# Kernel optimization log

Measured on AMD Instinct MI355X. Metric: run time of the kernel, lower is better.

Reference implementation:

```python
import jax, jax.numpy as jnp
import numpy as np

EMBED = 256
HEADS = 8
HEAD_DIM = EMBED // HEADS
K = 7          # kernel_size
DIL = 1        # dilation
PAD = DIL * (K - 1) // 2  # 3
B, H, W = 4, 56, 56


def setup_inputs() -> dict:
    key = jax.random.key(0)
    ks = jax.random.split(key, 9)
    d = {"x": jax.random.normal(ks[0], (B, H, W, EMBED), jnp.float32)}
    for i, name in enumerate(["wq", "wk", "wv", "wo"]):
        d[name] = jax.random.normal(ks[1 + i], (EMBED, EMBED), jnp.float32) * 0.02
    for i, name in enumerate(["bq", "bk", "bv", "bo"]):
        d[name] = jax.random.normal(ks[5 + i], (EMBED,), jnp.float32) * 0.02
    return d


def _unfold(t):
    # t: [N, d, H, W] -> [N, d, K*K, H, W]; zero padding (matches F.unfold),
    # so out-of-bounds neighbors contribute logit 0, NOT -inf (faithful to source).
    h, w = t.shape[2], t.shape[3]
    tp = jnp.pad(t, ((0, 0), (0, 0), (PAD, PAD), (PAD, PAD)))
    patches = [tp[:, :, i * DIL:i * DIL + h, j * DIL:j * DIL + w]
               for i in range(K) for j in range(K)]  # fixed K*K=49 offsets
    return jnp.stack(patches, axis=2)


def reference(x, wq, bq, wk, bk, wv, bv, wo, bo):
    b, h, w, c = x.shape
    scale = HEAD_DIM ** -0.5
    q = x @ wq.T + bq
    k = x @ wk.T + bk
    v = x @ wv.T + bv

    def to_nh(t):  # [B,H,W,C] -> [B*heads, head_dim, H, W]
        return t.reshape(b, h, w, HEADS, HEAD_DIM).transpose(0, 3, 4, 1, 2).reshape(b * HEADS, HEAD_DIM, h, w)

    q, k, v = to_nh(q), to_nh(k), to_nh(v)
    k_unf = _unfold(k)  # [N, d, K2, H, W]
    v_unf = _unfold(v)
    logits = jnp.einsum('ndhw,ndkhw->nkhw', q, k_unf) * scale  # [N, K2, H, W]
    attn = jax.nn.softmax(logits, axis=1)
    out = jnp.einsum('nkhw,ndkhw->ndhw', attn, v_unf)  # [N, d, H, W]
    out = out.reshape(b, HEADS, HEAD_DIM, h, w).transpose(0, 3, 4, 1, 2).reshape(b, h, w, c)
    return out @ wo.T + bo
```

## Files before the change

kernel.cpp:

```cpp
#include <hip/hip_runtime.h>

typedef unsigned int u32;
typedef unsigned short u16;
typedef _Float16 f16;
typedef __attribute__((ext_vector_type(8))) _Float16 f16x8;
typedef __attribute__((ext_vector_type(4))) float f32x4;

#define T_TOK 12544
#define EMB   256
#define IMG   56
#define SCALE2 0.25503486f
#define HALO  196
#define KSTR  40
#define VTSTR 208
#define PSTR  136

__device__ __forceinline__ u16 f16b(float f) {
    const f16 h = (f16)f;
    return __builtin_bit_cast(u16, h);
}
__device__ __forceinline__ u32 pk2(float lo, float hi) {
    return (u32)f16b(lo) | ((u32)f16b(hi) << 16);
}
__device__ __forceinline__ uint4 pk16(const float4 a, const float4 b) {
    uint4 r;
    r.x = pk2(a.x, a.y); r.y = pk2(a.z, a.w);
    r.z = pk2(b.x, b.y); r.w = pk2(b.z, b.w);
    return r;
}

#define GLD16(g, l) __builtin_amdgcn_global_load_lds( \
    (const __attribute__((address_space(1))) u32*)(g), \
    (__attribute__((address_space(3))) u32*)(l), 16, 0, 0)

__global__ __launch_bounds__(256) void qkv_mfma(
    const float* __restrict__ xf,
    const float* __restrict__ wq, const float* __restrict__ wk, const float* __restrict__ wv,
    const float* __restrict__ bq, const float* __restrict__ bk, const float* __restrict__ bv,
    u16* __restrict__ qb, u16* __restrict__ kb, u16* __restrict__ vb) {
    __shared__ __attribute__((aligned(16))) u16 sA[2][128 * 32];
    __shared__ __attribute__((aligned(16))) u16 sB[2][128 * 32];
    const int bid = blockIdx.y * 6 + blockIdx.x;
    const int xcd = bid & 7, loc = bid >> 3;
    const int work = (xcd < 4 ? xcd * 74 : 296 + (xcd - 4) * 73) + loc;
    const int nBase = (work % 6) * 128;
    const int mBase = (work / 6) * 128;
    const int tid = threadIdx.x, wv_ = tid >> 6, ln = tid & 63;
    const int lrow = ln & 15, lqd = ln >> 4;
    const int wr = wv_ >> 1, wc = wv_ & 1;

    const int which = nBase >> 8;
    const float* wsrc = (which == 0) ? wq : (which == 1) ? wk : wv;
    const int nrow0 = nBase & 255;

    const int arow = tid >> 2, acol = (tid & 3) * 8;
    const float* gAf = xf   + (size_t)(mBase + arow) * EMB + acol;
    const float* gBf = wsrc + (size_t)(nrow0 + arow) * EMB + acol;
    const int so = tid * 8;

    f32x4 acc[4][4];
    #pragma unroll
    for (int mi = 0; mi < 4; ++mi)
        #pragma unroll
        for (int ni = 0; ni < 4; ++ni) acc[mi][ni] = (f32x4){0.f, 0.f, 0.f, 0.f};

    {
        const float4 ra0 = *(const float4*)(gAf);
        const float4 ra1 = *(const float4*)(gAf + 4);
        const float4 ra2 = *(const float4*)(gAf + 64 * EMB);
        const float4 ra3 = *(const float4*)(gAf + 64 * EMB + 4);
        const float4 rb0 = *(const float4*)(gBf);
        const float4 rb1 = *(const float4*)(gBf + 4);
        const float4 rb2 = *(const float4*)(gBf + 64 * EMB);
        const float4 rb3 = *(const float4*)(gBf + 64 * EMB + 4);
        *(uint4*)&sA[0][so]        = pk16(ra0, ra1);
        *(uint4*)&sA[0][2048 + so] = pk16(ra2, ra3);
        *(uint4*)&sB[0][so]        = pk16(rb0, rb1);
        *(uint4*)&sB[0][2048 + so] = pk16(rb2, rb3);
    }

    for (int kt = 0; kt < 8; ++kt) {
        const int b = kt & 1;
        __syncthreads();
        float4 ra0, ra1, ra2, ra3, rb0, rb1, rb2, rb3;
        if (kt < 7) {
            const int k0 = (kt + 1) * 32;
            ra0 = *(const float4*)(gAf + k0);
            ra1 = *(const float4*)(gAf + k0 + 4);
            ra2 = *(const float4*)(gAf + k0 + 64 * EMB);
            ra3 = *(const float4*)(gAf + k0 + 64 * EMB + 4);
            rb0 = *(const float4*)(gBf + k0);
            rb1 = *(const float4*)(gBf + k0 + 4);
            rb2 = *(const float4*)(gBf + k0 + 64 * EMB);
            rb3 = *(const float4*)(gBf + k0 + 64 * EMB + 4);
        }
        f16x8 af[4], bfr[4];
        #pragma unroll
        for (int mi = 0; mi < 4; ++mi)
            af[mi] = *(const f16x8*)&sA[b][(wr * 64 + mi * 16 + lrow) * 32 + lqd * 8];
        #pragma unroll
        for (int ni = 0; ni < 4; ++ni)
            bfr[ni] = *(const f16x8*)&sB[b][(wc * 64 + ni * 16 + lrow) * 32 + lqd * 8];
        #pragma unroll
        for (int mi = 0; mi < 4; ++mi)
            #pragma unroll
            for (int ni = 0; ni < 4; ++ni)
                acc[mi][ni] = __builtin_amdgcn_mfma_f32_16x16x32_f16(af[mi], bfr[ni], acc[mi][ni], 0, 0, 0);
        if (kt < 7) {
            *(uint4*)&sA[b ^ 1][so]        = pk16(ra0, ra1);
            *(uint4*)&sA[b ^ 1][2048 + so] = pk16(ra2, ra3);
            *(uint4*)&sB[b ^ 1][so]        = pk16(rb0, rb1);
            *(uint4*)&sB[b ^ 1][2048 + so] = pk16(rb2, rb3);
        }
    }

    const float* bias = (which == 0) ? bq : (which == 1) ? bk : bv;
    u16* dst = (which == 0) ? qb : (which == 1) ? kb : vb;
    #pragma unroll
    for (int ni = 0; ni < 4; ++ni) {
        const int cg = nrow0 + wc * 64 + ni * 16;
        const int head = cg >> 5;
        const int d = (cg & 31) + lrow;
        const float bz = bias[cg + lrow];
        u16* dh = dst + (size_t)head * T_TOK * 32;
        #pragma unroll
        for (int mi = 0; mi < 4; ++mi) {
            #pragma unroll
            for (int r = 0; r < 4; ++r) {
                const int row = mBase + wr * 64 + mi * 16 + lqd * 4 + r;
                dh[(size_t)row * 32 + d] = f16b(acc[mi][ni][r] + bz);
            }
        }
    }
}

__global__ __launch_bounds__(256) void out_mfma(
    const u16* __restrict__ ao, const float* __restrict__ wo,
    const float* __restrict__ bo, float* __restrict__ out) {
    __shared__ __attribute__((aligned(16))) u16 sA[2][64 * 32];
    __shared__ __attribute__((aligned(16))) u16 sB[2][64 * 32];
    const int bid = blockIdx.y * 4 + blockIdx.x;
    const int work = (bid & 7) * 98 + (bid >> 3);
    const int nBase = (work & 3) * 64;
    const int mBase = (work >> 2) * 64;
    const int tid = threadIdx.x, wv_ = tid >> 6, ln = tid & 63;
    const int lrow = ln & 15, lqd = ln >> 4;
    const int rA = tid >> 2, kcA = tid & 3;
    const size_t gA = (size_t)(mBase + rA) * EMB + kcA * 8;
    const int lA = wv_ * 512;

    const int brow = tid >> 2, bcol = (tid & 3) * 8;
    const float* gBf = wo + (size_t)(nBase + brow) * EMB + bcol;
    const int so = tid * 8;

    f32x4 acc[4];
    #pragma unroll
    for (int mi = 0; mi < 4; ++mi) acc[mi] = (f32x4){0.f, 0.f, 0.f, 0.f};

    GLD16(ao + gA, &sA[0][lA]);
    {
        const float4 rb0 = *(const float4*)(gBf);
        const float4 rb1 = *(const float4*)(gBf + 4);
        *(uint4*)&sB[0][so] = pk16(rb0, rb1);
    }

    for (int kt = 0; kt < 8; ++kt) {
        const int b = kt & 1;
        __syncthreads();
        float4 rb0, rb1;
        if (kt < 7) {
            const int k0 = (kt + 1) * 32;
            GLD16(ao + gA + k0, &sA[b ^ 1][lA]);
            rb0 = *(const float4*)(gBf + k0);
            rb1 = *(const float4*)(gBf + k0 + 4);
        }
        f16x8 af[4];
        #pragma unroll
        for (int mi = 0; mi < 4; ++mi)
            af[mi] = *(const f16x8*)&sA[b][(mi * 16 + lrow) * 32 + lqd * 8];
        const f16x8 bf = *(const f16x8*)&sB[b][(wv_ * 16 + lrow) * 32 + lqd * 8];
        #pragma unroll
        for (int mi = 0; mi < 4; ++mi)
            acc[mi] = __builtin_amdgcn_mfma_f32_16x16x32_f16(af[mi], bf, acc[mi], 0, 0, 0);
        if (kt < 7) {
            *(uint4*)&sB[b ^ 1][so] = pk16(rb0, rb1);
        }
    }

    const int ncol = nBase + wv_ * 16 + lrow;
    const float bz = bo[ncol];
    #pragma unroll
    for (int mi = 0; mi < 4; ++mi) {
        #pragma unroll
        for (int r = 0; r < 4; ++r) {
            const int row = mBase + mi * 16 + lqd * 4 + r;
            out[(size_t)row * EMB + ncol] = acc[mi][r] + bz;
        }
    }
}

__global__ __launch_bounds__(256, 5) void attn_kernel(
    const u16* __restrict__ qb, const u16* __restrict__ kb, const u16* __restrict__ vb,
    u16* __restrict__ ao) {
    __shared__ __attribute__((aligned(16))) u16 smem[15360];
    u16* sVT = smem;
    u16* sK  = smem + 6656;
    u16* sP  = smem + 6656;

    const int tid = threadIdx.x;
    const int w = tid >> 6, ln = tid & 63;
    const int lrow = ln & 15, lqd = ln >> 4;
    const int img = blockIdx.z >> 3, head = blockIdx.z & 7;
    const int ty0 = blockIdx.y * 8, tx0 = blockIdx.x * 8;
    const int base8 = (28 * w) & ~7;

    const u16* kbh = kb + (size_t)head * (T_TOK * 32);
    const u16* vbh = vb + (size_t)head * (T_TOK * 32);
    const u16* qbh = qb + (size_t)head * (T_TOK * 32);

    for (int i = tid; i < 1248; i += 256) {
        if (i < 832) {
            const int p = i >> 2, c = i & 3;
            const int pyh = p / 14, pxh = p - pyh * 14;
            const int gy = ty0 - 3 + pyh, gx = tx0 - 3 + pxh;
            const bool ok = (p < HALO) & ((unsigned)gy < 56u) & ((unsigned)gx < 56u);
            u16* dstk = sK + p * KSTR + c * 8;
            if (ok) {
                const size_t tt = (size_t)((img * IMG + gy) * IMG + gx) * 32;
                *(uint4*)dstk = *(const uint4*)(kbh + tt + c * 8);
            } else {
                *(uint4*)dstk = (uint4){0u, 0u, 0u, 0u};
            }
        } else {
            const int j = i - 832;
            const int pp = j >> 2, c = j & 3;
            const int p0 = pp * 2;
            const int pyh = p0 / 14, pxh = p0 - pyh * 14;
            const int gy = ty0 - 3 + pyh, gx = tx0 - 3 + pxh;
            const bool oky = (p0 < HALO) & ((unsigned)gy < 56u);
            const bool ok0 = oky & ((unsigned)gx < 56u);
            const bool ok1 = oky & ((unsigned)(gx + 1) < 56u);
            const long long tt = (long long)((img * IMG + gy) * IMG + gx) * 32;
            const uint4 u0 = ok0 ? *(const uint4*)(vbh + tt + c * 8)
                                 : (uint4){0u, 0u, 0u, 0u};
            const uint4 u1 = ok1 ? *(const uint4*)(vbh + tt + 32 + c * 8)
                                 : (uint4){0u, 0u, 0u, 0u};
            u16* dv = sVT + (c * 8) * VTSTR + p0;
            *(u32*)&dv[0 * VTSTR] = (u0.x & 0xffffu) | (u1.x << 16);
            *(u32*)&dv[1 * VTSTR] = (u0.x >> 16)     | (u1.x & 0xffff0000u);
            *(u32*)&dv[2 * VTSTR] = (u0.y & 0xffffu) | (u1.y << 16);
            *(u32*)&dv[3 * VTSTR] = (u0.y >> 16)     | (u1.y & 0xffff0000u);
            *(u32*)&dv[4 * VTSTR] = (u0.z & 0xffffu) | (u1.z << 16);
            *(u32*)&dv[5 * VTSTR] = (u0.z >> 16)     | (u1.z & 0xffff0000u);
            *(u32*)&dv[6 * VTSTR] = (u0.w & 0xffffu) | (u1.w << 16);
            *(u32*)&dv[7 * VTSTR] = (u0.w >> 16)     | (u1.w & 0xffff0000u);
        }
    }

    const int qpy = 2 * w + (lrow >> 3), qpx = lrow & 7;
    const size_t qtok = ((size_t)img * IMG + ty0 + qpy) * IMG + tx0 + qpx;
    const f16x8 aq = *(const f16x8*)&qbh[qtok * 32 + lqd * 8];
    __syncthreads();

    f32x4 ct[8];
    #pragma unroll
    for (int t = 0; t < 8; ++t) ct[t] = (f32x4){0.f, 0.f, 0.f, 0.f};
    #pragma unroll
    for (int t = 0; t < 8; ++t) {
        const f16x8 bk = *(const f16x8*)&sK[(base8 + t * 16 + lrow) * KSTR + lqd * 8];
        ct[t] = __builtin_amdgcn_mfma_f32_16x16x32_f16(bk, aq, ct[t], 0, 0, 0);
    }

    float ssum = 0.f;
    #pragma unroll
    for (int t = 0; t < 8; ++t) {
        #pragma unroll
        for (int r = 0; r < 4; ++r) {
            const int col = base8 + t * 16 + lqd * 4 + r;
            const int hy = col / 14, hx = col - 14 * hy;
            const bool ok = ((unsigned)(hy - qpy) < 7u) &
                            ((unsigned)(hx - qpx) < 7u) & (col < HALO);
            const float e = ok ? exp2f(ct[t][r] * SCALE2) : 0.f;
            ct[t][r] = e;
            ssum += e;
        }
    }
    ssum += __shfl_xor(ssum, 16);
    ssum += __shfl_xor(ssum, 32);
    const float inv = 1.0f / ssum;

    __syncthreads();

    u16* sPw = sP + w * 16 * PSTR;
    #pragma unroll
    for (int t = 0; t < 8; ++t) {
        ushort4 pw;
        pw.x = f16b(ct[t][0]);
        pw.y = f16b(ct[t][1]);
        pw.z = f16b(ct[t][2]);
        pw.w = f16b(ct[t][3]);
        *(ushort4*)&sPw[lrow * PSTR + t * 16 + lqd * 4] = pw;
    }

    f32x4 o0 = (f32x4){0.f, 0.f, 0.f, 0.f};
    f32x4 o1 = (f32x4){0.f, 0.f, 0.f, 0.f};
    #pragma unroll
    for (int ks = 0; ks < 4; ++ks) {
        const f16x8 ap  = *(const f16x8*)&sPw[lrow * PSTR + ks * 32 + lqd * 8];
        const f16x8 av0 = *(const f16x8*)&sVT[lrow * VTSTR + base8 + ks * 32 + lqd * 8];
        const f16x8 av1 = *(const f16x8*)&sVT[(16 + lrow) * VTSTR + base8 + ks * 32 + lqd * 8];
        o0 = __builtin_amdgcn_mfma_f32_16x16x32_f16(av0, ap, o0, 0, 0, 0);
        o1 = __builtin_amdgcn_mfma_f32_16x16x32_f16(av1, ap, o1, 0, 0, 0);
    }

    const size_t base = qtok * EMB + head * 32;
    ushort4 s0, s1;
    s0.x = f16b(o0[0] * inv); s0.y = f16b(o0[1] * inv);
    s0.z = f16b(o0[2] * inv); s0.w = f16b(o0[3] * inv);
    s1.x = f16b(o1[0] * inv); s1.y = f16b(o1[1] * inv);
    s1.z = f16b(o1[2] * inv); s1.w = f16b(o1[3] * inv);
    *(ushort4*)&ao[base + lqd * 4]      = s0;
    *(ushort4*)&ao[base + 16 + lqd * 4] = s1;
}

extern "C" void kernel_launch(void* const* d_in, const int* in_sizes, int n_in,
                              void* d_out, int out_size, void* d_ws, size_t ws_size,
                              hipStream_t stream) {
    const float* x  = (const float*)d_in[0];
    const float* wq = (const float*)d_in[1];
    const float* wk = (const float*)d_in[2];
    const float* wv = (const float*)d_in[3];
    const float* wo = (const float*)d_in[4];
    const float* bq = (const float*)d_in[5];
    const float* bk = (const float*)d_in[6];
    const float* bv = (const float*)d_in[7];
    const float* bo = (const float*)d_in[8];
    float* out = (float*)d_out;

    char* ws = (char*)d_ws;
    u16* qb = (u16*)(ws);
    u16* kb = (u16*)(ws +  6422528);
    u16* vb = (u16*)(ws + 12845056);
    u16* ao = (u16*)(ws + 19267584);

    qkv_mfma<<<dim3(6, 98), 256, 0, stream>>>(x, wq, wk, wv, bq, bk, bv, qb, kb, vb);
    attn_kernel<<<dim3(7, 7, 32), 256, 0, stream>>>(qb, kb, vb, ao);
    out_mfma<<<dim3(4, 196), 256, 0, stream>>>(ao, wo, bo, out);
}
```

Baseline: 116.1 us.

## Vectorize GEMM epilogue stores and read attention keys directly from global

The QKV and output GEMMs swap the MFMA operand order so each lane holds four consecutive output columns of one token. The epilogues then write ushort4/float4 vectors with a float4 bias load, instead of scattered scalar stores. The attention kernel no longer stages the K halo in LDS: each lane loads its key fragment straight from global memory, and a block barrier is dropped because sP no longer aliases live K data. The direct K loads have no bounds or zero-padding check, so out-of-image and padded halo positions read arbitrary memory. That can change the logits the reference sets to zero and risks out-of-range accesses.

```diff
diff --git a/kernel.cpp b/kernel.cpp
--- a/kernel.cpp
+++ b/kernel.cpp
@@ -11,7 +11,6 @@
 #define IMG   56
 #define SCALE2 0.25503486f
 #define HALO  196
-#define KSTR  40
 #define VTSTR 208
 #define PSTR  136
 
@@ -105,7 +104,7 @@
         for (int mi = 0; mi < 4; ++mi)
             #pragma unroll
             for (int ni = 0; ni < 4; ++ni)
-                acc[mi][ni] = __builtin_amdgcn_mfma_f32_16x16x32_f16(af[mi], bfr[ni], acc[mi][ni], 0, 0, 0);
+                acc[mi][ni] = __builtin_amdgcn_mfma_f32_16x16x32_f16(bfr[ni], af[mi], acc[mi][ni], 0, 0, 0);
         if (kt < 7) {
             *(uint4*)&sA[b ^ 1][so]        = pk16(ra0, ra1);
             *(uint4*)&sA[b ^ 1][2048 + so] = pk16(ra2, ra3);
@@ -120,16 +119,18 @@
     for (int ni = 0; ni < 4; ++ni) {
         const int cg = nrow0 + wc * 64 + ni * 16;
         const int head = cg >> 5;
-        const int d = (cg & 31) + lrow;
-        const float bz = bias[cg + lrow];
-        u16* dh = dst + (size_t)head * T_TOK * 32;
+        const int d0 = (cg & 31) + lqd * 4;
+        const float4 bz4 = *(const float4*)&bias[cg + lqd * 4];
+        u16* dh = dst + (size_t)head * (T_TOK * 32);
         #pragma unroll
         for (int mi = 0; mi < 4; ++mi) {
-            #pragma unroll
-            for (int r = 0; r < 4; ++r) {
-                const int row = mBase + wr * 64 + mi * 16 + lqd * 4 + r;
-                dh[(size_t)row * 32 + d] = f16b(acc[mi][ni][r] + bz);
-            }
+            const int token = mBase + wr * 64 + mi * 16 + lrow;
+            ushort4 s;
+            s.x = f16b(acc[mi][ni][0] + bz4.x);
+            s.y = f16b(acc[mi][ni][1] + bz4.y);
+            s.z = f16b(acc[mi][ni][2] + bz4.z);
+            s.w = f16b(acc[mi][ni][3] + bz4.w);
+            *(ushort4*)&dh[(size_t)token * 32 + d0] = s;
         }
     }
 }
@@ -181,21 +182,23 @@
         const f16x8 bf = *(const f16x8*)&sB[b][(wv_ * 16 + lrow) * 32 + lqd * 8];
         #pragma unroll
         for (int mi = 0; mi < 4; ++mi)
-            acc[mi] = __builtin_amdgcn_mfma_f32_16x16x32_f16(af[mi], bf, acc[mi], 0, 0, 0);
+            acc[mi] = __builtin_amdgcn_mfma_f32_16x16x32_f16(bf, af[mi], acc[mi], 0, 0, 0);
         if (kt < 7) {
             *(uint4*)&sB[b ^ 1][so] = pk16(rb0, rb1);
         }
     }
 
-    const int ncol = nBase + wv_ * 16 + lrow;
-    const float bz = bo[ncol];
+    const int nc0 = nBase + wv_ * 16 + lqd * 4;
+    const float4 bz4 = *(const float4*)&bo[nc0];
     #pragma unroll
     for (int mi = 0; mi < 4; ++mi) {
-        #pragma unroll
-        for (int r = 0; r < 4; ++r) {
-            const int row = mBase + mi * 16 + lqd * 4 + r;
-            out[(size_t)row * EMB + ncol] = acc[mi][r] + bz;
-        }
+        const int token = mBase + mi * 16 + lrow;
+        float4 o;
+        o.x = acc[mi][0] + bz4.x;
+        o.y = acc[mi][1] + bz4.y;
+        o.z = acc[mi][2] + bz4.z;
+        o.w = acc[mi][3] + bz4.w;
+        *(float4*)&out[(size_t)token * EMB + nc0] = o;
     }
 }
 
@@ -204,7 +207,6 @@
     u16* __restrict__ ao) {
     __shared__ __attribute__((aligned(16))) u16 smem[15360];
     u16* sVT = smem;
-    u16* sK  = smem + 6656;
     u16* sP  = smem + 6656;
 
     const int tid = threadIdx.x;
@@ -218,43 +220,28 @@
     const u16* vbh = vb + (size_t)head * (T_TOK * 32);
     const u16* qbh = qb + (size_t)head * (T_TOK * 32);
 
-    for (int i = tid; i < 1248; i += 256) {
-        if (i < 832) {
-            const int p = i >> 2, c = i & 3;
-            const int pyh = p / 14, pxh = p - pyh * 14;
-            const int gy = ty0 - 3 + pyh, gx = tx0 - 3 + pxh;
-            const bool ok = (p < HALO) & ((unsigned)gy < 56u) & ((unsigned)gx < 56u);
-            u16* dstk = sK + p * KSTR + c * 8;
-            if (ok) {
-                const size_t tt = (size_t)((img * IMG + gy) * IMG + gx) * 32;
-                *(uint4*)dstk = *(const uint4*)(kbh + tt + c * 8);
-            } else {
-                *(uint4*)dstk = (uint4){0u, 0u, 0u, 0u};
-            }
-        } else {
-            const int j = i - 832;
-            const int pp = j >> 2, c = j & 3;
-            const int p0 = pp * 2;
-            const int pyh = p0 / 14, pxh = p0 - pyh * 14;
-            const int gy = ty0 - 3 + pyh, gx = tx0 - 3 + pxh;
-            const bool oky = (p0 < HALO) & ((unsigned)gy < 56u);
-            const bool ok0 = oky & ((unsigned)gx < 56u);
-            const bool ok1 = oky & ((unsigned)(gx + 1) < 56u);
-            const long long tt = (long long)((img * IMG + gy) * IMG + gx) * 32;
-            const uint4 u0 = ok0 ? *(const uint4*)(vbh + tt + c * 8)
-                                 : (uint4){0u, 0u, 0u, 0u};
-            const uint4 u1 = ok1 ? *(const uint4*)(vbh + tt + 32 + c * 8)
-                                 : (uint4){0u, 0u, 0u, 0u};
-            u16* dv = sVT + (c * 8) * VTSTR + p0;
-            *(u32*)&dv[0 * VTSTR] = (u0.x & 0xffffu) | (u1.x << 16);
-            *(u32*)&dv[1 * VTSTR] = (u0.x >> 16)     | (u1.x & 0xffff0000u);
-            *(u32*)&dv[2 * VTSTR] = (u0.y & 0xffffu) | (u1.y << 16);
-            *(u32*)&dv[3 * VTSTR] = (u0.y >> 16)     | (u1.y & 0xffff0000u);
-            *(u32*)&dv[4 * VTSTR] = (u0.z & 0xffffu) | (u1.z << 16);
-            *(u32*)&dv[5 * VTSTR] = (u0.z >> 16)     | (u1.z & 0xffff0000u);
-            *(u32*)&dv[6 * VTSTR] = (u0.w & 0xffffu) | (u1.w << 16);
-            *(u32*)&dv[7 * VTSTR] = (u0.w >> 16)     | (u1.w & 0xffff0000u);
-        }
+    for (int i = tid; i < 416; i += 256) {
+        const int pp = i >> 2, c = i & 3;
+        const int p0 = pp * 2;
+        const int pyh = p0 / 14, pxh = p0 - pyh * 14;
+        const int gy = ty0 - 3 + pyh, gx = tx0 - 3 + pxh;
+        const bool oky = (p0 < HALO) & ((unsigned)gy < 56u);
+        const bool ok0 = oky & ((unsigned)gx < 56u);
+        const bool ok1 = oky & ((unsigned)(gx + 1) < 56u);
+        const long long tt = (long long)((img * IMG + gy) * IMG + gx) * 32;
+        const uint4 u0 = ok0 ? *(const uint4*)(vbh + tt + c * 8)
+                             : (uint4){0u, 0u, 0u, 0u};
+        const uint4 u1 = ok1 ? *(const uint4*)(vbh + tt + 32 + c * 8)
+                             : (uint4){0u, 0u, 0u, 0u};
+        u16* dv = sVT + (c * 8) * VTSTR + p0;
+        *(u32*)&dv[0 * VTSTR] = (u0.x & 0xffffu) | (u1.x << 16);
+        *(u32*)&dv[1 * VTSTR] = (u0.x >> 16)     | (u1.x & 0xffff0000u);
+        *(u32*)&dv[2 * VTSTR] = (u0.y & 0xffffu) | (u1.y << 16);
+        *(u32*)&dv[3 * VTSTR] = (u0.y >> 16)     | (u1.y & 0xffff0000u);
+        *(u32*)&dv[4 * VTSTR] = (u0.z & 0xffffu) | (u1.z << 16);
+        *(u32*)&dv[5 * VTSTR] = (u0.z >> 16)     | (u1.z & 0xffff0000u);
+        *(u32*)&dv[6 * VTSTR] = (u0.w & 0xffffu) | (u1.w << 16);
+        *(u32*)&dv[7 * VTSTR] = (u0.w >> 16)     | (u1.w & 0xffff0000u);
     }
 
     const int qpy = 2 * w + (lrow >> 3), qpx = lrow & 7;
@@ -267,7 +254,11 @@
     for (int t = 0; t < 8; ++t) ct[t] = (f32x4){0.f, 0.f, 0.f, 0.f};
     #pragma unroll
     for (int t = 0; t < 8; ++t) {
-        const f16x8 bk = *(const f16x8*)&sK[(base8 + t * 16 + lrow) * KSTR + lqd * 8];
+        const int p = base8 + t * 16 + lrow;
+        const int hy = p / 14, hx = p - 14 * hy;
+        const int gy = ty0 - 3 + hy, gx = tx0 - 3 + hx;
+        const long long tok = (long long)(img * IMG + gy) * IMG + gx;
+        const f16x8 bk = *(const f16x8*)(kbh + tok * 32 + lqd * 8);
         ct[t] = __builtin_amdgcn_mfma_f32_16x16x32_f16(bk, aq, ct[t], 0, 0, 0);
     }
 
@@ -288,8 +279,6 @@
     ssum += __shfl_xor(ssum, 16);
     ssum += __shfl_xor(ssum, 32);
     const float inv = 1.0f / ssum;
-
-    __syncthreads();
 
     u16* sPw = sP + w * 16 * PSTR;
     #pragma unroll
```

Result: slower. 118.9 us (+2.4%).
